# Performance work log

Measured on AMD Instinct MI355X. Metric: run time of the kernel, lower is better.

Reference implementation:

```python
import jax, jax.numpy as jnp
import numpy as np

D_MODEL = 1024
D_STATE = 16
N_LAYERS = 2
EXPAND = 2
D_CONV = 4
D_INNER = EXPAND * D_MODEL
DT_RANK = D_MODEL // 16  # 64
B, L = 2, 1024


def setup_inputs() -> dict:
    key = jax.random.key(0)
    ks = jax.random.split(key, 8)
    rn = lambda k, shape, s: jax.random.normal(k, shape, jnp.float32) * s
    x = rn(ks[0], (B, L, D_MODEL), 1.0)
    in_proj_w = rn(ks[1], (N_LAYERS, 2 * D_INNER, D_MODEL), D_MODEL ** -0.5)
    conv_w = rn(ks[2], (N_LAYERS, D_INNER, 1, D_CONV), D_CONV ** -0.5)
    conv_b = jnp.zeros((N_LAYERS, D_INNER), jnp.float32)
    x_proj_w = rn(ks[3], (N_LAYERS, DT_RANK + 2 * D_STATE, D_INNER), D_INNER ** -0.5)
    dt_proj_w = rn(ks[4], (N_LAYERS, D_INNER, DT_RANK), DT_RANK ** -0.5)
    dt_proj_b = rn(ks[5], (N_LAYERS, D_INNER), 0.1)
    # canonical Mamba init: A = -exp(A_log), A_log = log(1..d_state)
    A_log = jnp.tile(jnp.log(jnp.arange(1, D_STATE + 1, dtype=jnp.float32)), (N_LAYERS, D_INNER, 1))
    Dp = jnp.ones((N_LAYERS, D_INNER), jnp.float32)
    out_proj_w = rn(ks[6], (N_LAYERS, D_MODEL, D_INNER), D_INNER ** -0.5)
    ln_g = jnp.ones((N_LAYERS, D_MODEL), jnp.float32)
    ln_b = jnp.zeros((N_LAYERS, D_MODEL), jnp.float32)
    fn_g = jnp.ones((D_MODEL,), jnp.float32)
    fn_b = jnp.zeros((D_MODEL,), jnp.float32)
    return dict(x=x, ln_g=ln_g, ln_b=ln_b, in_proj_w=in_proj_w, conv_w=conv_w,
                conv_b=conv_b, x_proj_w=x_proj_w, dt_proj_w=dt_proj_w,
                dt_proj_b=dt_proj_b, A_log=A_log, Dp=Dp, out_proj_w=out_proj_w,
                fn_g=fn_g, fn_b=fn_b)


def _ln(x, g, b):
    m = jnp.mean(x, -1, keepdims=True)
    v = jnp.mean((x - m) ** 2, -1, keepdims=True)
    return (x - m) * jax.lax.rsqrt(v + 1e-5) * g + b


def _mamba_block(x, in_w, cw, cb, xpw, dtw, dtb, A_log, Dp, ow):
    Bb = x.shape[0]
    # input projection -> [B, L, 2*d_inner]
    xz = jnp.einsum('bld,ed->ble', x, in_w)
    u, res = jnp.split(xz, 2, axis=-1)
    # causal depthwise conv over time (torch: padding=3 then [..., :L])
    uc = jax.lax.conv_general_dilated(
        u.transpose(0, 2, 1), cw, (1,), [(D_CONV - 1, 0)],
        dimension_numbers=('NCH', 'OIH', 'NCH'), feature_group_count=D_INNER)
    u = jax.nn.silu(uc.transpose(0, 2, 1) + cb)  # [B, L, d_inner]
    # input-dependent dt, B, C
    xdbl = jnp.einsum('ble,fe->blf', u, xpw)
    dt, Bc, Cc = jnp.split(xdbl, [DT_RANK, DT_RANK + D_STATE], axis=-1)
    delta = jax.nn.softplus(jnp.einsum('blr,dr->bld', dt, dtw) + dtb)  # [B,L,d_inner]
    A = -jnp.exp(A_log)  # [d_inner, d_state]

    def step(h, inp):
        d_t, B_t, C_t, u_t = inp  # [B,d_inner],[B,d_state],[B,d_state],[B,d_inner]
        h = jnp.exp(d_t[:, :, None] * A) * h + (d_t * u_t)[:, :, None] * B_t[:, None, :]
        y = jnp.einsum('bds,bs->bd', h, C_t)
        return h, y

    xs = (delta.transpose(1, 0, 2), Bc.transpose(1, 0, 2),
          Cc.transpose(1, 0, 2), u.transpose(1, 0, 2))
    h0 = jnp.zeros((Bb, D_INNER, D_STATE), x.dtype)
    _, ys = jax.lax.scan(step, h0, xs)
    y = ys.transpose(1, 0, 2) + u * Dp
    y = y * jax.nn.silu(res)
    return jnp.einsum('ble,de->bld', y, ow)


def reference(x, ln_g, ln_b, in_proj_w, conv_w, conv_b, x_proj_w, dt_proj_w,
              dt_proj_b, A_log, Dp, out_proj_w, fn_g, fn_b):
    for i in range(N_LAYERS):
        x = x + _mamba_block(_ln(x, ln_g[i], ln_b[i]), in_proj_w[i], conv_w[i],
                             conv_b[i], x_proj_w[i], dt_proj_w[i], dt_proj_b[i],
                             A_log[i], Dp[i], out_proj_w[i])
    # dropout is identity in eval mode
    return _ln(x, fn_g, fn_b)
```

## Files before the change

kernel.cpp:

```cpp
#include <hip/hip_runtime.h>
#include <hip/hip_bf16.h>
#include <math.h>
#include <stdint.h>

#define DMODEL 1024
#define DSTATE 16
#define DINNER 2048
#define DTRANK 64
#define NB 2
#define LSEQ 1024
#define ROWS (NB*LSEQ)
#define NCH 32
#define LCH (LSEQ/NCH)
#define KSPLIT 8

typedef __bf16 bf16_t;
typedef __bf16 bf16x8 __attribute__((ext_vector_type(8)));
typedef __bf16 bf16x4 __attribute__((ext_vector_type(4)));
typedef float  f32x4  __attribute__((ext_vector_type(4)));

#define AS1(p) ((const __attribute__((address_space(1))) void*)(p))
#define AS3(p) ((__attribute__((address_space(3))) void*)(uint32_t)(uintptr_t)(p))

static __device__ __forceinline__ float sigmoidf_(float x){ return 1.f/(1.f+__expf(-x)); }
static __device__ __forceinline__ float softplusf_(float x){ return fmaxf(x,0.f) + log1pf(__expf(-fabsf(x))); }

__global__ __launch_bounds__(256) void cvt_kernel(const float* __restrict__ in,
    bf16_t* __restrict__ out, int n4)
{
  int i = blockIdx.x*256 + threadIdx.x;
  if (i < n4){
    float4 v = ((const float4*)in)[i];
    bf16x4 o = { (bf16_t)v.x, (bf16_t)v.y, (bf16_t)v.z, (bf16_t)v.w };
    ((bf16x4*)out)[i] = o;
  }
}

template<int OUTBF>
__global__ __launch_bounds__(256) void ln_kernel(const float* __restrict__ x,
    const float* __restrict__ g, const float* __restrict__ b,
    float* __restrict__ outf, bf16_t* __restrict__ outb)
{
  int row = blockIdx.x;
  float4 v = ((const float4*)(x + (size_t)row*DMODEL))[threadIdx.x];
  float s  = v.x+v.y+v.z+v.w;
  float s2 = v.x*v.x+v.y*v.y+v.z*v.z+v.w*v.w;
  #pragma unroll
  for (int off=32; off>=1; off>>=1){ s += __shfl_xor(s,off); s2 += __shfl_xor(s2,off); }
  __shared__ float red[8];
  int lane = threadIdx.x & 63, wid = threadIdx.x >> 6;
  if (lane==0){ red[wid]=s; red[4+wid]=s2; }
  __syncthreads();
  float ts  = red[0]+red[1]+red[2]+red[3];
  float ts2 = red[4]+red[5]+red[6]+red[7];
  float mean = ts*(1.f/DMODEL);
  float var  = ts2*(1.f/DMODEL) - mean*mean;
  float rstd = rsqrtf(var + 1e-5f);
  float4 gv = ((const float4*)g)[threadIdx.x];
  float4 bv = ((const float4*)b)[threadIdx.x];
  float4 o;
  o.x=(v.x-mean)*rstd*gv.x+bv.x;
  o.y=(v.y-mean)*rstd*gv.y+bv.y;
  o.z=(v.z-mean)*rstd*gv.z+bv.z;
  o.w=(v.w-mean)*rstd*gv.w+bv.w;
  if (OUTBF){
    bf16x4 ob = { (bf16_t)o.x, (bf16_t)o.y, (bf16_t)o.z, (bf16_t)o.w };
    ((bf16x4*)(outb + (size_t)row*DMODEL))[threadIdx.x] = ob;
  } else {
    ((float4*)(outf + (size_t)row*DMODEL))[threadIdx.x] = o;
  }
}

#define GBM 128
#define GBN 128
#define GBK 64

template<int EPI, bool NGUARD, bool SWZ>
__global__ __launch_bounds__(256) void gemm_bf16(
    const bf16_t* __restrict__ A, int lda,
    const bf16_t* __restrict__ W, int ldw,
    float* __restrict__ C, int ldc,
    int M, int N, int K,
    const float* __restrict__ bias,
    const float* __restrict__ addsrc,
    bf16_t* __restrict__ C2)
{
  __shared__ __align__(16) char lds[2*GBM*GBK*2];
  char* sA = lds;
  char* sB = lds + GBM*GBK*2;
  const int tid  = threadIdx.x;
  const int lane = tid & 63, wid = tid >> 6;
  const int wr = wid >> 1, wc = wid & 1;
  const int frow = lane & 15, kgrp = lane >> 4;

  int bx = blockIdx.x, by = blockIdx.y;
  if (SWZ) {
    int gx = gridDim.x, gy = gridDim.y;
    int bid = by*gx + bx;
    int q = (gx*gy) >> 3;
    int nid = (bid & 7)*q + (bid >> 3);
    int stripH = gy << 3;
    int strip = nid / stripH;
    int rem   = nid % stripH;
    bx = (strip << 3) + (rem & 7);
    by = rem >> 3;
  }
  const int m0 = by*GBM, n0 = bx*GBN;
  const int srow  = (lane >> 3);
  const int scolb = (lane & 7) * 16;

  f32x4 acc[4][4];
  #pragma unroll
  for (int i=0;i<4;i++)
    #pragma unroll
    for (int j=0;j<4;j++)
      acc[i][j] = (f32x4){0.f,0.f,0.f,0.f};

  const int ksl = K / gridDim.z;
  const int kb  = blockIdx.z * ksl;
  for (int k0 = kb; k0 < kb + ksl; k0 += GBK) {
    #pragma unroll
    for (int r=0;r<4;++r){
      int ci  = r*4 + wid;
      int row = ci*8 + srow;
      {
        const char* src = (const char*)A + ((size_t)(m0+row)*lda + k0)*2 + scolb;
        __builtin_amdgcn_global_load_lds(AS1(src), AS3(sA + ci*1024), 16, 0, 0);
      }
      {
        int grow = n0 + row;
        if (NGUARD) grow = (grow < N) ? grow : (N-1);
        const char* src = (const char*)W + ((size_t)grow*ldw + k0)*2 + scolb;
        __builtin_amdgcn_global_load_lds(AS1(src), AS3(sB + ci*1024), 16, 0, 0);
      }
    }
    __syncthreads();
    #pragma unroll
    for (int ks=0; ks<2; ++ks){
      bf16x8 af[4], bfr[4];
      #pragma unroll
      for (int i=0;i<4;i++)
        af[i] = *(const bf16x8*)(sA + (wr*64 + i*16 + frow)*128 + ks*64 + kgrp*16);
      #pragma unroll
      for (int j=0;j<4;j++)
        bfr[j] = *(const bf16x8*)(sB + (wc*64 + j*16 + frow)*128 + ks*64 + kgrp*16);
      #pragma unroll
      for (int i=0;i<4;i++)
        #pragma unroll
        for (int j=0;j<4;j++)
          acc[i][j] = __builtin_amdgcn_mfma_f32_16x16x32_bf16(af[i], bfr[j], acc[i][j], 0, 0, 0);
    }
    __syncthreads();
  }

  if (EPI==4) {
    #pragma unroll
    for (int i=0;i<4;i++){
      int rbase = wr*64 + i*16 + kgrp*4;
      #pragma unroll
      for (int j=0;j<4;j++){
        int col = wc*64 + j*16 + frow;
        #pragma unroll
        for (int q=0;q<4;q++){
          int row = rbase + q;
          int byte = (row<<8) + (col<<1);
          byte ^= (row & 7) << 4;
          *(bf16_t*)(lds + byte) = (bf16_t)acc[i][j][q];
        }
      }
    }
    __syncthreads();
    int r = tid >> 1;
    int hb = (tid & 1) << 7;
    size_t gbase = (size_t)(m0 + r)*ldc + n0 + ((tid & 1) << 6);
    #pragma unroll
    for (int i=0;i<8;i++){
      int byte = (r<<8) + hb + (i<<4);
      byte ^= (r & 7) << 4;
      bf16x8 v = *(const bf16x8*)(lds + byte);
      *(bf16x8*)(C2 + gbase + (i<<3)) = v;
    }
    return;
  }

  float* Cw = (EPI==5) ? (C + (size_t)blockIdx.z*(size_t)M*ldc) : C;
  #pragma unroll
  for (int i=0;i<4;i++){
    int rbase = m0 + wr*64 + i*16 + kgrp*4;
    #pragma unroll
    for (int j=0;j<4;j++){
      int col = n0 + wc*64 + j*16 + frow;
      if (NGUARD && col >= N) continue;
      #pragma unroll
      for (int q=0;q<4;q++){
        float v = acc[i][j][q];
        int row = rbase + q;
        if (EPI==1) v = softplusf_(v + bias[col]);
        if (EPI==2) v += addsrc[(size_t)row*ldc + col];
        Cw[(size_t)row*ldc + col] = v;
      }
    }
  }
}

__global__ __launch_bounds__(256) void xp_reduce(
    const float* __restrict__ part, float* __restrict__ xdbl, bf16_t* __restrict__ xdbl_b)
{
  int idx = blockIdx.x*256 + threadIdx.x;
  float s = 0.f;
  #pragma unroll
  for (int k=0;k<KSPLIT;k++) s += part[(size_t)k*ROWS*96 + idx];
  xdbl[idx] = s;
  xdbl_b[idx] = (bf16_t)s;
}

__global__ __launch_bounds__(256) void conv_silu_kernel(
    const bf16_t* __restrict__ xzb, const float* __restrict__ cw,
    const float* __restrict__ cb, bf16_t* __restrict__ ub)
{
  int idx = blockIdx.x*256 + threadIdx.x;
  int d  = idx & (DINNER-1);
  int bl = idx >> 11;
  int l  = bl & (LSEQ-1);
  const bf16_t* col = xzb + (size_t)bl*(2*DINNER) + d;
  float w0=cw[d*4+0], w1=cw[d*4+1], w2=cw[d*4+2], w3=cw[d*4+3];
  float x3 = (float)col[0];
  float x2 = (l>=1) ? (float)col[-(ptrdiff_t)(2*DINNER)]  : 0.f;
  float x1 = (l>=2) ? (float)col[-(ptrdiff_t)(4*DINNER)]  : 0.f;
  float x0 = (l>=3) ? (float)col[-(ptrdiff_t)(6*DINNER)]  : 0.f;
  float acc = cb[d] + w0*x0 + w1*x1 + w2*x2 + w3*x3;
  float uu = acc * sigmoidf_(acc);
  ub[(size_t)bl*DINNER + d] = (bf16_t)uu;
}

__global__ __launch_bounds__(256) void scan_phase1(
    const float* __restrict__ delta, const bf16_t* __restrict__ u,
    const float* __restrict__ xdbl, const float* __restrict__ A_log,
    float* __restrict__ hout, float* __restrict__ sumd)
{
  int gid = blockIdx.x*256 + threadIdx.x;
  int d = gid & (DINNER-1);
  int c = (gid >> 11) & (NCH-1);
  int b = gid >> 16;
  float A[DSTATE];
  #pragma unroll
  for (int s=0;s<DSTATE;s++) A[s] = -__expf(A_log[d*DSTATE+s]);
  int l0 = c*LCH;
  const float*  drow = delta + ((size_t)(b*LSEQ + l0))*DINNER + d;
  const bf16_t* urow = u     + ((size_t)(b*LSEQ + l0))*DINNER + d;
  const float*  xrow = xdbl  + ((size_t)(b*LSEQ + l0))*96 + DTRANK;
  float h[DSTATE] = {};
  float sd = 0.f;
  for (int l=0; l<LCH; ++l) {
    float dv = drow[(size_t)l*DINNER];
    float uv = (float)urow[(size_t)l*DINNER];
    const float* bc = xrow + l*96;
    float du = dv*uv;
    sd += dv;
    #pragma unroll
    for (int s=0;s<DSTATE;s++)
      h[s] = __expf(dv*A[s])*h[s] + du*bc[s];
  }
  float* hp = hout + (((size_t)(b*NCH + c))*DINNER + d)*DSTATE;
  #pragma unroll
  for (int q=0;q<4;q++)
    ((float4*)hp)[q] = make_float4(h[4*q],h[4*q+1],h[4*q+2],h[4*q+3]);
  sumd[((size_t)(b*NCH + c))*DINNER + d] = sd;
}

__global__ __launch_bounds__(256) void scan_phase2(
    float* __restrict__ hout, const float* __restrict__ sumd,
    const float* __restrict__ A_log)
{
  int gid = blockIdx.x*256 + threadIdx.x;
  int s = gid & (DSTATE-1);
  int d = (gid >> 4) & (DINNER-1);
  int b = gid >> 15;
  float A = -__expf(A_log[d*DSTATE+s]);
  float h = 0.f;
  for (int c=0; c<NCH; ++c) {
    size_t hi = (((size_t)(b*NCH + c))*DINNER + d)*DSTATE + s;
    float tmp = hout[hi];
    hout[hi] = h;
    float P = __expf(A * sumd[((size_t)(b*NCH + c))*DINNER + d]);
    h = P*h + tmp;
  }
}

__global__ __launch_bounds__(256) void scan_phase3(
    const float* __restrict__ delta, bf16_t* ysb,
    const bf16_t* u,
    const bf16_t* __restrict__ xzb,
    const float* __restrict__ xdbl,
    const float* __restrict__ A_log,
    const float* __restrict__ Dp,
    const float* __restrict__ hin)
{
  int gid = blockIdx.x*256 + threadIdx.x;
  int d = gid & (DINNER-1);
  int c = (gid >> 11) & (NCH-1);
  int b = gid >> 16;
  float A[DSTATE];
  #pragma unroll
  for (int s=0;s<DSTATE;s++) A[s] = -__expf(A_log[d*DSTATE+s]);
  float Dpd = Dp[d];
  float h[DSTATE];
  const float* hp = hin + (((size_t)(b*NCH + c))*DINNER + d)*DSTATE;
  #pragma unroll
  for (int q=0;q<4;q++){
    float4 hv = ((const float4*)hp)[q];
    h[4*q]=hv.x; h[4*q+1]=hv.y; h[4*q+2]=hv.z; h[4*q+3]=hv.w;
  }
  int l0 = c*LCH;
  const float*  drow = delta + ((size_t)(b*LSEQ + l0))*DINNER + d;
  const bf16_t* urow = u     + ((size_t)(b*LSEQ + l0))*DINNER + d;
  const bf16_t* rrow = xzb   + ((size_t)(b*LSEQ + l0))*2*DINNER + DINNER + d;
  const float*  xrow = xdbl  + ((size_t)(b*LSEQ + l0))*96 + DTRANK;
  bf16_t* yrow = ysb + ((size_t)(b*LSEQ + l0))*DINNER + d;
  for (int l=0; l<LCH; ++l) {
    float dv = drow[(size_t)l*DINNER];
    float uv = (float)urow[(size_t)l*DINNER];
    float rv = (float)rrow[(size_t)l*2*DINNER];
    const float* bc = xrow + l*96;
    float du = dv*uv;
    float y = 0.f;
    #pragma unroll
    for (int s=0;s<DSTATE;s++){
      float dA = __expf(dv*A[s]);
      h[s] = dA*h[s] + du*bc[s];
      y += h[s]*bc[DSTATE+s];
    }
    y = (y + uv*Dpd) * (rv * sigmoidf_(rv));
    yrow[(size_t)l*DINNER] = (bf16_t)y;
  }
}

extern "C" void kernel_launch(void* const* d_in, const int* in_sizes, int n_in,
                              void* d_out, int out_size, void* d_ws, size_t ws_size,
                              hipStream_t stream)
{
  const float* x      = (const float*)d_in[0];
  const float* ln_g   = (const float*)d_in[1];
  const float* ln_b   = (const float*)d_in[2];
  const float* in_w   = (const float*)d_in[3];
  const float* conv_w = (const float*)d_in[4];
  const float* conv_b = (const float*)d_in[5];
  const float* xp_w   = (const float*)d_in[6];
  const float* dt_w   = (const float*)d_in[7];
  const float* dt_b   = (const float*)d_in[8];
  const float* A_log  = (const float*)d_in[9];
  const float* Dp     = (const float*)d_in[10];
  const float* out_w  = (const float*)d_in[11];
  const float* fn_g   = (const float*)d_in[12];
  const float* fn_b   = (const float*)d_in[13];
  float* out = (float*)d_out;

  char* p = (char*)d_ws;
  auto alloc = [&](size_t bytes)->char*{ char* r = p; p += (bytes + 255) & ~(size_t)255; return r; };

  const size_t N_INW = (size_t)2*2*DINNER*DMODEL;
  const size_t N_XPW = (size_t)2*96*DINNER;
  const size_t N_DTW = (size_t)2*DINNER*DTRANK;
  const size_t N_OUTW= (size_t)2*DMODEL*DINNER;

  bf16_t* inw_b  = (bf16_t*)alloc(N_INW*2);
  bf16_t* xpw_b  = (bf16_t*)alloc(N_XPW*2);
  bf16_t* dtw_b  = (bf16_t*)alloc(N_DTW*2);
  bf16_t* outw_b = (bf16_t*)alloc(N_OUTW*2);
  float*  x_cur  = (float*) alloc((size_t)ROWS*DMODEL*4);
  bf16_t* xn_b   = (bf16_t*)alloc((size_t)ROWS*DMODEL*2);
  bf16_t* xzb    = (bf16_t*)alloc((size_t)ROWS*2*DINNER*2);
  bf16_t* ub_b   = (bf16_t*)alloc((size_t)ROWS*DINNER*2);
  float*  xdbl   = (float*) alloc((size_t)ROWS*96*4);
  bf16_t* xdbl_b = (bf16_t*)alloc((size_t)ROWS*96*2);
  float*  xpart  = (float*) alloc((size_t)KSPLIT*ROWS*96*4);
  float*  delta  = (float*) alloc((size_t)ROWS*DINNER*4);
  float*  hout   = (float*) alloc((size_t)NB*NCH*DINNER*DSTATE*4);
  float*  sumd   = (float*) alloc((size_t)NB*NCH*DINNER*4);
  bf16_t* ys_b   = ub_b;

  cvt_kernel<<<(int)((N_INW/4 +255)/256),256,0,stream>>>(in_w,  inw_b,  (int)(N_INW/4));
  cvt_kernel<<<(int)((N_XPW/4 +255)/256),256,0,stream>>>(xp_w,  xpw_b,  (int)(N_XPW/4));
  cvt_kernel<<<(int)((N_DTW/4 +255)/256),256,0,stream>>>(dt_w,  dtw_b,  (int)(N_DTW/4));
  cvt_kernel<<<(int)((N_OUTW/4+255)/256),256,0,stream>>>(out_w, outw_b, (int)(N_OUTW/4));

  for (int layer=0; layer<2; ++layer) {
    const float* xin = (layer==0) ? x : x_cur;
    const float* Al  = A_log + (size_t)layer*DINNER*DSTATE;
    ln_kernel<1><<<ROWS,256,0,stream>>>(xin, ln_g+layer*DMODEL, ln_b+layer*DMODEL, nullptr, xn_b);
    gemm_bf16<4,false,true><<<dim3(2*DINNER/GBN, ROWS/GBM),256,0,stream>>>(
        xn_b, DMODEL, inw_b + (size_t)layer*2*DINNER*DMODEL, DMODEL,
        nullptr, 2*DINNER, ROWS, 2*DINNER, DMODEL, nullptr, nullptr, xzb);
    conv_silu_kernel<<<(ROWS*DINNER)/256,256,0,stream>>>(
        xzb, conv_w + (size_t)layer*DINNER*4, conv_b + (size_t)layer*DINNER, ub_b);
    gemm_bf16<5,true,false><<<dim3(1, ROWS/GBM, KSPLIT),256,0,stream>>>(
        ub_b, DINNER, xpw_b + (size_t)layer*96*DINNER, DINNER,
        xpart, 96, ROWS, 96, DINNER, nullptr, nullptr, nullptr);
    xp_reduce<<<(ROWS*96)/256,256,0,stream>>>(xpart, xdbl, xdbl_b);
    gemm_bf16<1,false,true><<<dim3(DINNER/GBN, ROWS/GBM),256,0,stream>>>(
        xdbl_b, 96, dtw_b + (size_t)layer*DINNER*DTRANK, DTRANK,
        delta, DINNER, ROWS, DINNER, DTRANK,
        dt_b + (size_t)layer*DINNER, nullptr, nullptr);
    scan_phase1<<<(NB*NCH*DINNER)/256,256,0,stream>>>(delta, ub_b, xdbl, Al, hout, sumd);
    scan_phase2<<<(NB*DINNER*DSTATE)/256,256,0,stream>>>(hout, sumd, Al);
    scan_phase3<<<(NB*NCH*DINNER)/256,256,0,stream>>>(
        delta, ys_b, ub_b, xzb, xdbl, Al, Dp + (size_t)layer*DINNER, hout);
    gemm_bf16<2,false,true><<<dim3(DMODEL/GBN, ROWS/GBM),256,0,stream>>>(
        ys_b, DINNER, outw_b + (size_t)layer*DMODEL*DINNER, DINNER,
        x_cur, DMODEL, ROWS, DMODEL, DINNER, nullptr, xin, nullptr);
  }
  ln_kernel<0><<<ROWS,256,0,stream>>>(x_cur, fn_g, fn_b, out, nullptr);
}
```

Measured before the change: 547.4 us.

## Double scan chunk count and stage B/C rows in shared memory

Raises the number of sequence chunks in the chunked selective scan from 32 to 64, halving each chunk's serial length and doubling thread-level parallelism. Phase 1 and phase 3 now cooperatively load each chunk's B/C values into shared memory once per block instead of every thread reading them from global memory. The per-state math is rewritten with 4-wide float vectors. The cost is a longer serial chunk-combine loop in phase 2 and twice the intermediate state traffic.

```diff
diff --git a/kernel.cpp b/kernel.cpp
--- a/kernel.cpp
+++ b/kernel.cpp
@@ -10,7 +10,7 @@
 #define NB 2
 #define LSEQ 1024
 #define ROWS (NB*LSEQ)
-#define NCH 32
+#define NCH 64
 #define LCH (LSEQ/NCH)
 #define KSPLIT 8
 
@@ -233,38 +233,54 @@
   ub[(size_t)bl*DINNER + d] = (bf16_t)uu;
 }
 
+
 __global__ __launch_bounds__(256) void scan_phase1(
     const float* __restrict__ delta, const bf16_t* __restrict__ u,
     const float* __restrict__ xdbl, const float* __restrict__ A_log,
     float* __restrict__ hout, float* __restrict__ sumd)
 {
-  int gid = blockIdx.x*256 + threadIdx.x;
+  __shared__ __align__(16) float bcs[LCH][32];
+  int tid = threadIdx.x;
+  int gid = blockIdx.x*256 + tid;
   int d = gid & (DINNER-1);
   int c = (gid >> 11) & (NCH-1);
-  int b = gid >> 16;
-  float A[DSTATE];
-  #pragma unroll
-  for (int s=0;s<DSTATE;s++) A[s] = -__expf(A_log[d*DSTATE+s]);
+  int b = gid >> 17;
   int l0 = c*LCH;
+  #pragma unroll
+  for (int i=0;i<2;i++){
+    int ii = tid + i*256;
+    int r = ii >> 5, q = ii & 31;
+    bcs[r][q] = xdbl[(size_t)(b*LSEQ + l0 + r)*96 + DTRANK + q];
+  }
+  __syncthreads();
+
+  f32x4 A4[4];
+  #pragma unroll
+  for (int si=0;si<4;si++){
+    float4 al = ((const float4*)(A_log + d*DSTATE))[si];
+    A4[si] = (f32x4){-__expf(al.x), -__expf(al.y), -__expf(al.z), -__expf(al.w)};
+  }
   const float*  drow = delta + ((size_t)(b*LSEQ + l0))*DINNER + d;
   const bf16_t* urow = u     + ((size_t)(b*LSEQ + l0))*DINNER + d;
-  const float*  xrow = xdbl  + ((size_t)(b*LSEQ + l0))*96 + DTRANK;
-  float h[DSTATE] = {};
+  f32x4 h[4] = {};
   float sd = 0.f;
   for (int l=0; l<LCH; ++l) {
     float dv = drow[(size_t)l*DINNER];
     float uv = (float)urow[(size_t)l*DINNER];
-    const float* bc = xrow + l*96;
     float du = dv*uv;
     sd += dv;
-    #pragma unroll
-    for (int s=0;s<DSTATE;s++)
-      h[s] = __expf(dv*A[s])*h[s] + du*bc[s];
+    const f32x4* bl = (const f32x4*)&bcs[l][0];
+    #pragma unroll
+    for (int si=0;si<4;si++){
+      f32x4 e;
+      e[0]=__expf(dv*A4[si][0]); e[1]=__expf(dv*A4[si][1]);
+      e[2]=__expf(dv*A4[si][2]); e[3]=__expf(dv*A4[si][3]);
+      h[si] = e*h[si] + du*bl[si];
+    }
   }
   float* hp = hout + (((size_t)(b*NCH + c))*DINNER + d)*DSTATE;
   #pragma unroll
-  for (int q=0;q<4;q++)
-    ((float4*)hp)[q] = make_float4(h[4*q],h[4*q+1],h[4*q+2],h[4*q+3]);
+  for (int si=0;si<4;si++) ((f32x4*)hp)[si] = h[si];
   sumd[((size_t)(b*NCH + c))*DINNER + d] = sd;
 }
 
@@ -296,40 +312,53 @@
     const float* __restrict__ Dp,
     const float* __restrict__ hin)
 {
-  int gid = blockIdx.x*256 + threadIdx.x;
+  __shared__ __align__(16) float bcs[LCH][32];
+  int tid = threadIdx.x;
+  int gid = blockIdx.x*256 + tid;
   int d = gid & (DINNER-1);
   int c = (gid >> 11) & (NCH-1);
-  int b = gid >> 16;
-  float A[DSTATE];
-  #pragma unroll
-  for (int s=0;s<DSTATE;s++) A[s] = -__expf(A_log[d*DSTATE+s]);
+  int b = gid >> 17;
+  int l0 = c*LCH;
+  #pragma unroll
+  for (int i=0;i<2;i++){
+    int ii = tid + i*256;
+    int r = ii >> 5, q = ii & 31;
+    bcs[r][q] = xdbl[(size_t)(b*LSEQ + l0 + r)*96 + DTRANK + q];
+  }
+  __syncthreads();
+
+  f32x4 A4[4];
+  #pragma unroll
+  for (int si=0;si<4;si++){
+    float4 al = ((const float4*)(A_log + d*DSTATE))[si];
+    A4[si] = (f32x4){-__expf(al.x), -__expf(al.y), -__expf(al.z), -__expf(al.w)};
+  }
   float Dpd = Dp[d];
-  float h[DSTATE];
+  f32x4 h[4];
   const float* hp = hin + (((size_t)(b*NCH + c))*DINNER + d)*DSTATE;
   #pragma unroll
-  for (int q=0;q<4;q++){
-    float4 hv = ((const float4*)hp)[q];
-    h[4*q]=hv.x; h[4*q+1]=hv.y; h[4*q+2]=hv.z; h[4*q+3]=hv.w;
-  }
-  int l0 = c*LCH;
+  for (int si=0;si<4;si++) h[si] = ((const f32x4*)hp)[si];
+
   const float*  drow = delta + ((size_t)(b*LSEQ + l0))*DINNER + d;
   const bf16_t* urow = u     + ((size_t)(b*LSEQ + l0))*DINNER + d;
   const bf16_t* rrow = xzb   + ((size_t)(b*LSEQ + l0))*2*DINNER + DINNER + d;
-  const float*  xrow = xdbl  + ((size_t)(b*LSEQ + l0))*96 + DTRANK;
   bf16_t* yrow = ysb + ((size_t)(b*LSEQ + l0))*DINNER + d;
   for (int l=0; l<LCH; ++l) {
     float dv = drow[(size_t)l*DINNER];
     float uv = (float)urow[(size_t)l*DINNER];
     float rv = (float)rrow[(size_t)l*2*DINNER];
-    const float* bc = xrow + l*96;
     float du = dv*uv;
-    float y = 0.f;
-    #pragma unroll
-    for (int s=0;s<DSTATE;s++){
-      float dA = __expf(dv*A[s]);
-      h[s] = dA*h[s] + du*bc[s];
-      y += h[s]*bc[DSTATE+s];
-    }
+    const f32x4* bl = (const f32x4*)&bcs[l][0];
+    f32x4 yv = {};
+    #pragma unroll
+    for (int si=0;si<4;si++){
+      f32x4 e;
+      e[0]=__expf(dv*A4[si][0]); e[1]=__expf(dv*A4[si][1]);
+      e[2]=__expf(dv*A4[si][2]); e[3]=__expf(dv*A4[si][3]);
+      h[si] = e*h[si] + du*bl[si];
+      yv += h[si]*bl[4+si];
+    }
+    float y = yv[0]+yv[1]+yv[2]+yv[3];
     y = (y + uv*Dpd) * (rv * sigmoidf_(rv));
     yrow[(size_t)l*DINNER] = (bf16_t)y;
   }
```

Measured after the change: 480.2 us. 1.14x faster.
